# Kernel tuning notes

Hardware: AMD Instinct MI355X
Metric: run time of the kernel (lower is better)

## Reference

```python
import jax, jax.numpy as jnp
import numpy as np

SR = 48000
MAX_DUR = 5.0
N_AUDIO = 480000  # 10 s @ 48 kHz
K_IR = int(SR * MAX_DUR)  # 240000 taps


def setup_inputs() -> dict:
    key = jax.random.key(0)
    k1, k2 = jax.random.split(key)
    audio = jax.random.normal(k1, (N_AUDIO,), dtype=jnp.float32)
    impulse_response = jax.random.normal(k2, (K_IR,), dtype=jnp.float32)
    return {"audio": audio, "impulse_response": impulse_response}


def reference(audio, impulse_response):
    # torch: pad audio with (K-1) zeros, then conv1d (= cross-correlation, no flip)
    K = impulse_response.shape[0]
    a_pad = jnp.concatenate([audio, jnp.zeros((K - 1,), dtype=audio.dtype)])
    # out[t] = sum_k a_pad[t+k] * ir[k], valid correlation -> length N
    out = jnp.correlate(a_pad, impulse_response, mode="valid")
    # trailing peak normalization
    return out / jnp.max(jnp.abs(out))
```

## Files before the change

### kernel.cpp

```cpp
#include <hip/hip_runtime.h>

typedef unsigned int u32;


constexpr int N_AUDIO = 480000;
constexpr int K_IR    = 240000;
constexpr int M_FFT   = 1048576;

constexpr size_t OFF_C0   = 0;
constexpr size_t OFF_C1   = (size_t)M_FFT * 8;
constexpr size_t OFF_SLOT = OFF_C1 + (size_t)M_FFT * 8;

#define SW(i) ((i) + ((i) >> 4))
constexpr int LSZ = 1088;

__device__ __forceinline__ float2 cmul(float2 a, float2 b) {
    return make_float2(a.x * b.x - a.y * b.y, a.x * b.y + a.y * b.x);
}
__device__ __forceinline__ float2 twid(float frac) {
    float s, c;
    __sincosf(-6.28318530717958647692f * frac, &s, &c);
    return make_float2(c, s);
}
__device__ __forceinline__ void build_tw(float2* tw, int t) {
    #pragma unroll
    for (int i = t + 1; i < 1024; i += 256) {
        int L = 1 << (31 - __builtin_clz(i));
        tw[i] = twid((float)(i - L) / (float)(2 * L));
    }
}

template<int NB>
__device__ __forceinline__ void fft1024_r4(float2 (*A0)[LSZ], float2 (*B0)[LSZ],
                                           const float2* tw, int t) {
    float2 (*A)[LSZ] = A0;
    float2 (*B)[LSZ] = B0;
    #pragma unroll
    for (int s = 0; s < 5; ++s) {
        const int L  = 1 << (2 * s);
        const int k  = t & (L - 1);
        const int p0 = 4 * t - 3 * k;
        const float2 w  = tw[L + k];
        const float2 w2 = tw[2 * L + k];
        #pragma unroll
        for (int j = 0; j < NB; ++j) {
            float2 x0 = A[j][SW(t)];
            float2 x2 = A[j][SW(t + 256)];
            float2 x1 = A[j][SW(t + 512)];
            float2 x3 = A[j][SW(t + 768)];
            float2 wx1 = cmul(w, x1), wx3 = cmul(w, x3);
            float2 u0 = make_float2(x0.x + wx1.x, x0.y + wx1.y);
            float2 u1 = make_float2(x0.x - wx1.x, x0.y - wx1.y);
            float2 u2 = make_float2(x2.x + wx3.x, x2.y + wx3.y);
            float2 u3 = make_float2(x2.x - wx3.x, x2.y - wx3.y);
            float2 a2 = cmul(w2, u2);
            float2 a3 = cmul(w2, u3);
            B[j][SW(p0)]         = make_float2(u0.x + a2.x, u0.y + a2.y);
            B[j][SW(p0 + L)]     = make_float2(u1.x + a3.y, u1.y - a3.x);
            B[j][SW(p0 + 2*L)]   = make_float2(u0.x - a2.x, u0.y - a2.y);
            B[j][SW(p0 + 3*L)]   = make_float2(u1.x - a3.y, u1.y + a3.x);
        }
        __syncthreads();
        float2 (*tmp)[LSZ] = A; A = B; B = tmp;
    }
}

__global__ __launch_bounds__(256) void fft1_p1(const float* __restrict__ a,
                                               const float* __restrict__ b,
                                               float2* __restrict__ outb,
                                               u32* __restrict__ slot) {
    __shared__ float2 rows[1][LSZ], scr[1][LSZ], tw[1024];
    const int t = threadIdx.x;
    const int r = blockIdx.x;
    if (r == 0 && t == 0) *slot = 0u;
    build_tw(tw, t);
    #pragma unroll
    for (int q = 0; q < 4; ++q) {
        int c = t + 256 * q;
        int idx = c * 1024 + r;
        float av = (idx < N_AUDIO) ? a[idx] : 0.0f;
        float bv = (idx < K_IR)    ? b[idx] : 0.0f;
        rows[0][SW(c)] = make_float2(av, bv);
    }
    __syncthreads();
    fft1024_r4<1>(rows, scr, tw, t);
    const float fr = (float)r * (1.0f / 1048576.0f);
    #pragma unroll
    for (int q = 0; q < 4; ++q) {
        int k1 = t + 256 * q;
        outb[r * 1024 + k1] = cmul(twid(fr * (float)k1), scr[0][SW(k1)]);
    }
}

__global__ __launch_bounds__(256) void fft1_p2_pw(const float2* __restrict__ in,
                                                  float2* __restrict__ spec) {
    __shared__ float2 cols[2][LSZ], scr[2][LSZ], tw[1024];
    const int t = threadIdx.x;
    const int bidx = blockIdx.x;
    const int cA = (bidx == 0) ? 0   : bidx;
    const int cB = (bidx == 0) ? 512 : 1024 - bidx;
    build_tw(tw, t);
    #pragma unroll
    for (int q = 0; q < 4; ++q) {
        int r = t + 256 * q;
        cols[0][SW(r)] = in[r * 1024 + cA];
        cols[1][SW(r)] = in[r * 1024 + cB];
    }
    __syncthreads();
    fft1024_r4<2>(cols, scr, tw, t);
    const float invM = 1.0f / 1048576.0f;
    #pragma unroll
    for (int q = 0; q < 4; ++q) {
        int k2 = t + 256 * q;
        #pragma unroll
        for (int j = 0; j < 2; ++j) {
            float2 z1 = scr[j][SW(k2)];
            float2 z2;
            if (bidx == 0) z2 = (j == 0) ? scr[0][SW((1024 - k2) & 1023)]
                                         : scr[1][SW(1023 - k2)];
            else           z2 = scr[j ^ 1][SW(1023 - k2)];
            float2 Af  = make_float2(0.5f * (z1.x + z2.x), 0.5f * (z1.y - z2.y));
            float2 cBf = make_float2(0.5f * (z1.y + z2.y), 0.5f * (z1.x - z2.x));
            float2 S   = cmul(Af, cBf);
            int cc = (j == 0) ? cA : cB;
            spec[cc * 1024 + k2] = make_float2(S.x * invM, -S.y * invM);
        }
    }
}

__global__ __launch_bounds__(256) void fft2_p1(const float2* __restrict__ in,
                                               float2* __restrict__ outb) {
    __shared__ float2 rows[1][LSZ], scr[1][LSZ], tw[1024];
    const int t = threadIdx.x;
    const int r = blockIdx.x;
    build_tw(tw, t);
    #pragma unroll
    for (int q = 0; q < 4; ++q) {
        int c = t + 256 * q;
        rows[0][SW(c)] = in[r * 1024 + c];
    }
    __syncthreads();
    fft1024_r4<1>(rows, scr, tw, t);
    const float fr = (float)r * (1.0f / 1048576.0f);
    #pragma unroll
    for (int q = 0; q < 4; ++q) {
        int k1 = t + 256 * q;
        outb[r * 1024 + k1] = cmul(twid(fr * (float)k1), scr[0][SW(k1)]);
    }
}

__global__ __launch_bounds__(256) void fft2_p2(const float2* __restrict__ in,
                                               float* __restrict__ raw,
                                               u32* __restrict__ slot) {
    __shared__ float2 cols[1][LSZ], scr[1][LSZ], tw[1024];
    __shared__ float wmax[4];
    const int t = threadIdx.x;
    const int c = blockIdx.x;
    build_tw(tw, t);
    #pragma unroll
    for (int q = 0; q < 4; ++q) {
        int r = t + 256 * q;
        cols[0][SW(r)] = in[r * 1024 + c];
    }
    __syncthreads();
    fft1024_r4<1>(cols, scr, tw, t);
    float m = 0.0f;
    #pragma unroll
    for (int q = 0; q < 4; ++q) {
        int k2 = t + 256 * q;
        int ot = c + (k2 << 10);
        if (ot < N_AUDIO) {
            float v = scr[0][SW(k2)].x;
            raw[ot] = v;
            m = fmaxf(m, fabsf(v));
        }
    }
    for (int off = 32; off > 0; off >>= 1) m = fmaxf(m, __shfl_down(m, off, 64));
    if ((t & 63) == 0) wmax[t >> 6] = m;
    __syncthreads();
    if (t == 0) {
        float bm = fmaxf(fmaxf(wmax[0], wmax[1]), fmaxf(wmax[2], wmax[3]));
        atomicMax(slot, __float_as_uint(bm));
    }
}

__global__ __launch_bounds__(256) void scale_k(const float* __restrict__ raw,
                                               const u32* __restrict__ slot,
                                               float* __restrict__ out) {
    int i = blockIdx.x * 256 + threadIdx.x;
    if (i < N_AUDIO) out[i] = raw[i] / __uint_as_float(*slot);
}

extern "C" void kernel_launch(void* const* d_in, const int* in_sizes, int n_in,
                              void* d_out, int out_size, void* d_ws, size_t ws_size,
                              hipStream_t stream) {
    const float* audio = (const float*)d_in[0];
    const float* ir    = (const float*)d_in[1];
    float* out = (float*)d_out;

    char* ws = (char*)d_ws;
    float2* cb0 = (float2*)(ws + OFF_C0);
    float2* cb1 = (float2*)(ws + OFF_C1);
    u32*    slot = (u32*)(ws + OFF_SLOT);

    fft1_p1<<<1024, 256, 0, stream>>>(audio, ir, cb1, slot);
    fft1_p2_pw<<<512, 256, 0, stream>>>(cb1, cb0);
    fft2_p1<<<1024, 256, 0, stream>>>(cb0, cb1);
    fft2_p2<<<1024, 256, 0, stream>>>(cb1, (float*)cb0, slot);
    scale_k<<<1875, 256, 0, stream>>>((const float*)cb0, slot, out);
}
```

Measured before the change: 115.0 us.

## Precompute twiddle ROM tables, batch two FFT rows per block, vectorize loads, transpose output

Replaces the per-block sincos twiddle generation with compile-time constant tables, and builds the large inter-pass twiddles as a product of two entries from those tables. Each FFT kernel now handles two rows or columns per block, so global loads can be float2/float4 wide and the grid is half as large. The second pass writes its output in a transposed layout that coalesces better, and the scale kernel reads it through a shared-memory tile transpose. The trade-offs are more shared memory per block, which can lower occupancy, and fewer blocks in flight.

```diff
diff --git a/kernel.cpp b/kernel.cpp
--- a/kernel.cpp
+++ b/kernel.cpp
@@ -14,25 +14,50 @@
 #define SW(i) ((i) + ((i) >> 4))
 constexpr int LSZ = 1088;
 
+struct F2 { float x, y; };
+constexpr double D_PI = 3.14159265358979323846264338327950288;
+constexpr double tay_sin(double x) {
+    double t = x, s = x, x2 = x * x;
+    for (int k = 1; k <= 11; ++k) { t *= -x2 / (double)((2 * k) * (2 * k + 1)); s += t; }
+    return s;
+}
+constexpr double tay_cos(double x) {
+    double t = 1.0, s = 1.0, x2 = x * x;
+    for (int k = 1; k <= 11; ++k) { t *= -x2 / (double)((2 * k - 1) * (2 * k)); s += t; }
+    return s;
+}
+struct Tab { F2 v[1024]; };
+constexpr Tab make_t1() {
+    Tab tb{};
+    for (int j = 0; j < 1024; ++j) {
+        int jj = (j < 512) ? j : j - 1024;
+        double a = -2.0 * D_PI * (double)jj / 1024.0;
+        tb.v[j] = F2{(float)tay_cos(a), (float)tay_sin(a)};
+    }
+    return tb;
+}
+constexpr Tab make_t2() {
+    Tab tb{};
+    for (int j = 0; j < 1024; ++j) {
+        double a = -2.0 * D_PI * (double)j / 1048576.0;
+        tb.v[j] = F2{(float)tay_cos(a), (float)tay_sin(a)};
+    }
+    return tb;
+}
+__device__ constexpr Tab ROM_T1 = make_t1();
+__device__ constexpr Tab ROM_T2 = make_t2();
+
+__device__ __forceinline__ float2 ldrom(const Tab& tb, int i) {
+    F2 f = tb.v[i];
+    return make_float2(f.x, f.y);
+}
 __device__ __forceinline__ float2 cmul(float2 a, float2 b) {
     return make_float2(a.x * b.x - a.y * b.y, a.x * b.y + a.y * b.x);
 }
-__device__ __forceinline__ float2 twid(float frac) {
-    float s, c;
-    __sincosf(-6.28318530717958647692f * frac, &s, &c);
-    return make_float2(c, s);
-}
-__device__ __forceinline__ void build_tw(float2* tw, int t) {
-    #pragma unroll
-    for (int i = t + 1; i < 1024; i += 256) {
-        int L = 1 << (31 - __builtin_clz(i));
-        tw[i] = twid((float)(i - L) / (float)(2 * L));
-    }
-}
 
 template<int NB>
 __device__ __forceinline__ void fft1024_r4(float2 (*A0)[LSZ], float2 (*B0)[LSZ],
-                                           const float2* tw, int t) {
+                                           const float2* lt1, int t) {
     float2 (*A)[LSZ] = A0;
     float2 (*B)[LSZ] = B0;
     #pragma unroll
@@ -40,8 +65,8 @@
         const int L  = 1 << (2 * s);
         const int k  = t & (L - 1);
         const int p0 = 4 * t - 3 * k;
-        const float2 w  = tw[L + k];
-        const float2 w2 = tw[2 * L + k];
+        const float2 w  = lt1[k << (9 - 2 * s)];
+        const float2 w2 = lt1[k << (8 - 2 * s)];
         #pragma unroll
         for (int j = 0; j < NB; ++j) {
             float2 x0 = A[j][SW(t)];
@@ -69,37 +94,49 @@
                                                const float* __restrict__ b,
                                                float2* __restrict__ outb,
                                                u32* __restrict__ slot) {
-    __shared__ float2 rows[1][LSZ], scr[1][LSZ], tw[1024];
-    const int t = threadIdx.x;
-    const int r = blockIdx.x;
-    if (r == 0 && t == 0) *slot = 0u;
-    build_tw(tw, t);
+    __shared__ float2 rows[2][LSZ], scr[2][LSZ], lt1[1024], lt2[1024];
+    const int t  = threadIdx.x;
+    const int r0 = blockIdx.x * 2;
+    if (blockIdx.x == 0 && t == 0) *slot = 0u;
+    #pragma unroll
+    for (int q = 0; q < 4; ++q) {
+        int i = t + 256 * q;
+        lt1[i] = ldrom(ROM_T1, i);
+        lt2[i] = ldrom(ROM_T2, i);
+    }
     #pragma unroll
     for (int q = 0; q < 4; ++q) {
         int c = t + 256 * q;
-        int idx = c * 1024 + r;
-        float av = (idx < N_AUDIO) ? a[idx] : 0.0f;
-        float bv = (idx < K_IR)    ? b[idx] : 0.0f;
-        rows[0][SW(c)] = make_float2(av, bv);
-    }
-    __syncthreads();
-    fft1024_r4<1>(rows, scr, tw, t);
-    const float fr = (float)r * (1.0f / 1048576.0f);
+        int base = c * 1024 + r0;
+        float2 av = make_float2(0.f, 0.f), bv = make_float2(0.f, 0.f);
+        if (c < 468 || (c == 468 && r0 < 768)) av = *(const float2*)(a + base);
+        if (c < 234 || (c == 234 && r0 < 384)) bv = *(const float2*)(b + base);
+        rows[0][SW(c)] = make_float2(av.x, bv.x);
+        rows[1][SW(c)] = make_float2(av.y, bv.y);
+    }
+    __syncthreads();
+    fft1024_r4<2>(rows, scr, lt1, t);
     #pragma unroll
     for (int q = 0; q < 4; ++q) {
         int k1 = t + 256 * q;
-        outb[r * 1024 + k1] = cmul(twid(fr * (float)k1), scr[0][SW(k1)]);
+        #pragma unroll
+        for (int j = 0; j < 2; ++j) {
+            int e = (r0 + j) * k1;
+            float2 w = cmul(lt1[e >> 10], lt2[e & 1023]);
+            outb[(r0 + j) * 1024 + k1] = cmul(w, scr[j][SW(k1)]);
+        }
     }
 }
 
 __global__ __launch_bounds__(256) void fft1_p2_pw(const float2* __restrict__ in,
                                                   float2* __restrict__ spec) {
-    __shared__ float2 cols[2][LSZ], scr[2][LSZ], tw[1024];
+    __shared__ float2 cols[2][LSZ], scr[2][LSZ], lt1[1024];
     const int t = threadIdx.x;
     const int bidx = blockIdx.x;
     const int cA = (bidx == 0) ? 0   : bidx;
     const int cB = (bidx == 0) ? 512 : 1024 - bidx;
-    build_tw(tw, t);
+    #pragma unroll
+    for (int q = 0; q < 4; ++q) { int i = t + 256 * q; lt1[i] = ldrom(ROM_T1, i); }
     #pragma unroll
     for (int q = 0; q < 4; ++q) {
         int r = t + 256 * q;
@@ -107,7 +144,7 @@
         cols[1][SW(r)] = in[r * 1024 + cB];
     }
     __syncthreads();
-    fft1024_r4<2>(cols, scr, tw, t);
+    fft1024_r4<2>(cols, scr, lt1, t);
     const float invM = 1.0f / 1048576.0f;
     #pragma unroll
     for (int q = 0; q < 4; ++q) {
@@ -130,49 +167,68 @@
 
 __global__ __launch_bounds__(256) void fft2_p1(const float2* __restrict__ in,
                                                float2* __restrict__ outb) {
-    __shared__ float2 rows[1][LSZ], scr[1][LSZ], tw[1024];
-    const int t = threadIdx.x;
-    const int r = blockIdx.x;
-    build_tw(tw, t);
-    #pragma unroll
-    for (int q = 0; q < 4; ++q) {
-        int c = t + 256 * q;
-        rows[0][SW(c)] = in[r * 1024 + c];
-    }
-    __syncthreads();
-    fft1024_r4<1>(rows, scr, tw, t);
-    const float fr = (float)r * (1.0f / 1048576.0f);
+    __shared__ float2 rows[2][LSZ], scr[2][LSZ], lt1[1024], lt2[1024];
+    const int t  = threadIdx.x;
+    const int r0 = blockIdx.x * 2;
+    #pragma unroll
+    for (int q = 0; q < 4; ++q) {
+        int i = t + 256 * q;
+        lt1[i] = ldrom(ROM_T1, i);
+        lt2[i] = ldrom(ROM_T2, i);
+    }
+    const float4* inv4 = (const float4*)(in + (size_t)r0 * 1024);
+    #pragma unroll
+    for (int q = 0; q < 4; ++q) {
+        int i2 = t + 256 * q;
+        float4 v = inv4[i2];
+        int j = i2 >> 9, c = (i2 & 511) * 2;
+        rows[j][SW(c)]     = make_float2(v.x, v.y);
+        rows[j][SW(c + 1)] = make_float2(v.z, v.w);
+    }
+    __syncthreads();
+    fft1024_r4<2>(rows, scr, lt1, t);
     #pragma unroll
     for (int q = 0; q < 4; ++q) {
         int k1 = t + 256 * q;
-        outb[r * 1024 + k1] = cmul(twid(fr * (float)k1), scr[0][SW(k1)]);
+        #pragma unroll
+        for (int j = 0; j < 2; ++j) {
+            int e = (r0 + j) * k1;
+            float2 w = cmul(lt1[e >> 10], lt2[e & 1023]);
+            outb[(r0 + j) * 1024 + k1] = cmul(w, scr[j][SW(k1)]);
+        }
     }
 }
 
 __global__ __launch_bounds__(256) void fft2_p2(const float2* __restrict__ in,
-                                               float* __restrict__ raw,
+                                               float* __restrict__ rawT,
                                                u32* __restrict__ slot) {
-    __shared__ float2 cols[1][LSZ], scr[1][LSZ], tw[1024];
+    __shared__ float2 cols[2][LSZ], scr[2][LSZ], lt1[1024];
     __shared__ float wmax[4];
-    const int t = threadIdx.x;
-    const int c = blockIdx.x;
-    build_tw(tw, t);
+    const int t  = threadIdx.x;
+    const int c0 = blockIdx.x * 2;
+    #pragma unroll
+    for (int q = 0; q < 4; ++q) { int i = t + 256 * q; lt1[i] = ldrom(ROM_T1, i); }
     #pragma unroll
     for (int q = 0; q < 4; ++q) {
         int r = t + 256 * q;
-        cols[0][SW(r)] = in[r * 1024 + c];
-    }
-    __syncthreads();
-    fft1024_r4<1>(cols, scr, tw, t);
+        float4 v = *(const float4*)(in + (size_t)r * 1024 + c0);
+        cols[0][SW(r)] = make_float2(v.x, v.y);
+        cols[1][SW(r)] = make_float2(v.z, v.w);
+    }
+    __syncthreads();
+    fft1024_r4<2>(cols, scr, lt1, t);
     float m = 0.0f;
     #pragma unroll
     for (int q = 0; q < 4; ++q) {
         int k2 = t + 256 * q;
-        int ot = c + (k2 << 10);
-        if (ot < N_AUDIO) {
-            float v = scr[0][SW(k2)].x;
-            raw[ot] = v;
-            m = fmaxf(m, fabsf(v));
+        #pragma unroll
+        for (int j = 0; j < 2; ++j) {
+            int ot = c0 + j + (k2 << 10);
+            if (ot < N_AUDIO) {
+                float v = scr[j][SW(k2)].x;
+                rawT[(c0 + j) * 512 + k2] = v;
+                m = fmaxf(m, fabsf(v));
+            }
         }
     }
     for (int off = 32; off > 0; off >>= 1) m = fmaxf(m, __shfl_down(m, off, 64));
@@ -184,11 +240,31 @@
     }
 }
 
-__global__ __launch_bounds__(256) void scale_k(const float* __restrict__ raw,
+__global__ __launch_bounds__(256) void scale_t(const float* __restrict__ rawT,
                                                const u32* __restrict__ slot,
                                                float* __restrict__ out) {
-    int i = blockIdx.x * 256 + threadIdx.x;
-    if (i < N_AUDIO) out[i] = raw[i] / __uint_as_float(*slot);
+    __shared__ float tile[64][65];
+    const int t  = threadIdx.x;
+    const int c0 = (blockIdx.x & 15) * 64;
+    const int k0 = (blockIdx.x >> 4) * 64;
+    const int cl = t >> 2, ch = (t & 3) * 16;
+    #pragma unroll
+    for (int i = 0; i < 4; ++i) {
+        float4 v = *(const float4*)(rawT + (size_t)(c0 + cl) * 512 + k0 + ch + i * 4);
+        tile[cl][ch + i * 4 + 0] = v.x;
+        tile[cl][ch + i * 4 + 1] = v.y;
+        tile[cl][ch + i * 4 + 2] = v.z;
+        tile[cl][ch + i * 4 + 3] = v.w;
+    }
+    __syncthreads();
+    const float inv = 1.0f / __uint_as_float(*slot);
+    const int cw = t & 63, w = t >> 6;
+    #pragma unroll
+    for (int q = 0; q < 16; ++q) {
+        int kk = q * 4 + w;
+        int o = (k0 + kk) * 1024 + c0 + cw;
+        if (o < N_AUDIO) out[o] = tile[cw][kk] * inv;
+    }
 }
 
 extern "C" void kernel_launch(void* const* d_in, const int* in_sizes, int n_in,
@@ -203,9 +279,9 @@
     float2* cb1 = (float2*)(ws + OFF_C1);
     u32*    slot = (u32*)(ws + OFF_SLOT);
 
-    fft1_p1<<<1024, 256, 0, stream>>>(audio, ir, cb1, slot);
+    fft1_p1<<<512, 256, 0, stream>>>(audio, ir, cb1, slot);
     fft1_p2_pw<<<512, 256, 0, stream>>>(cb1, cb0);
-    fft2_p1<<<1024, 256, 0, stream>>>(cb0, cb1);
-    fft2_p2<<<1024, 256, 0, stream>>>(cb1, (float*)cb0, slot);
-    scale_k<<<1875, 256, 0, stream>>>((const float*)cb0, slot, out);
-}
+    fft2_p1<<<512, 256, 0, stream>>>(cb0, cb1);
+    fft2_p2<<<512, 256, 0, stream>>>(cb1, (float*)cb0, slot);
+    scale_t<<<128, 256, 0, stream>>>((const float*)cb0, slot, out);
+}
```

After: 109.4 us. 4.9% less time.
